# Optimization experiments

Measured on AMD Instinct MI355X. Metric: run time of the kernel, lower is better.

## Reference

```python
import jax, jax.numpy as jnp
import numpy as np

B, C, H, W = 4, 3, 96, 96
HW = H * W
IGNORE = 0          # HD_IGNORE_CLASS_INDEX
BIG = 1e9           # stand-in for +inf in masked min


def setup_inputs() -> dict:
    key = jax.random.key(0)
    k1, k2 = jax.random.split(key)
    predictions = jax.random.normal(k1, (B, C, H, W), dtype=jnp.float32)
    labels_int = jax.random.randint(k2, (B, H, W), 0, C, dtype=jnp.int32)
    return {"predictions": predictions, "labels_int": labels_int}


def get_boundary(img):
    # img: [B, C, H, W] binary mask. Faithful to the numpy version (square images):
    # new = img + 4-neighbor sums (zero outside), boundary = img * (5 - new).
    pad = lambda x, spec: jnp.pad(x, ((0, 0), (0, 0)) + spec)
    new = (img
           + pad(img[:, :, 1:, :], ((0, 1), (0, 0)))
           + pad(img[:, :, :-1, :], ((1, 0), (0, 0)))
           + pad(img[:, :, :, 1:], ((0, 0), (0, 1)))
           + pad(img[:, :, :, :-1], ((0, 0), (1, 0))))
    return img * (5.0 - new)


def _pixel_dist_matrix():
    yy, xx = jnp.meshgrid(jnp.arange(H), jnp.arange(W), indexing="ij")
    coords = jnp.stack([yy.ravel(), xx.ravel()], axis=-1).astype(jnp.float32)  # [HW,2] (row,col) like argwhere
    sq = jnp.sum(coords * coords, axis=-1)
    D2 = sq[:, None] + sq[None, :] - 2.0 * (coords @ coords.T)
    return jnp.sqrt(jnp.maximum(D2, 0.0))  # [HW, HW]


def reference(predictions, labels_int):
    labels = jax.nn.one_hot(labels_int, C, axis=1, dtype=jnp.float32)        # [B,C,H,W]
    preds = jax.nn.one_hot(jnp.argmax(predictions, axis=1), C, axis=1,
                           dtype=jnp.float32)                                # [B,C,H,W]

    bd_a = (get_boundary(preds) > 0).astype(jnp.float32)
    bd_b = (get_boundary(labels) > 0).astype(jnp.float32)

    a = preds.reshape(B * C, HW)
    b = labels.reshape(B * C, HW)
    ba = bd_a.reshape(B * C, HW)
    bb = bd_b.reshape(B * C, HW)

    D = _pixel_dist_matrix()  # [HW, HW], shared across all (batch, class) pairs

    def pair(args):
        a_, b_, ba_, bb_ = args
        n_a = a_.sum()
        n_b = b_.sum()
        a_fwd = a_ * (1.0 - b_)   # pred-only pixels (false positive region)
        b_bwd = b_ * (1.0 - a_)   # label-only pixels
        # min distance from every pixel to boundary set, via masked min (no argwhere)
        mins_f = jnp.min(jnp.where(bb_[None, :] > 0, D, BIG), axis=1)  # to boundary(b)
        mins_b = jnp.min(jnp.where(ba_[None, :] > 0, D, BIG), axis=1)  # to boundary(a)
        # mean(min) * |A_fwd| / |a| == sum(min over A_fwd) / |a|
        hd_f = jnp.where((a_fwd.sum() > 0) & (bb_.sum() > 0),
                         jnp.sum(a_fwd * mins_f) / jnp.maximum(n_a, 1.0), 0.0)
        hd_b = jnp.where((b_bwd.sum() > 0) & (ba_.sum() > 0),
                         jnp.sum(b_bwd * mins_b) / jnp.maximum(n_b, 1.0), 0.0)
        hd = jnp.maximum(hd_f, hd_b)
        # empty prediction mask -> failure case (ignore_failed_hd = False => (h+w)/4)
        hd = jnp.where(n_a > 0, hd, (H + W) / 4.0)
        return hd, (n_a == 0).astype(jnp.float32)

    hd_pairs, failed_pairs = jax.lax.map(pair, (a, b, ba, bb))

    hd = hd_pairs.reshape(B, C).at[:, IGNORE].set(0.0)
    failed = failed_pairs.reshape(B, C).sum(axis=0).at[IGNORE].set(0.0)

    HD = jnp.zeros((B, C + 2), dtype=jnp.float32)
    HD = HD.at[:, :C].set(hd)
    HD = HD.at[:, C].set(jnp.mean(hd, axis=1))            # HD[:, -2] = mean over all C classes
    HD = HD.at[:, C + 1].set(jnp.mean(hd[:, :C - 1], axis=1))  # HD[:, -1] = mean over first C-1 (faithful to [:-3])

    Fc = jnp.zeros((C + 2,), dtype=jnp.float32)
    Fc = Fc.at[:C].set(failed)
    Fc = Fc.at[C].set(jnp.mean(failed))
    Fc = Fc.at[C + 1].set(jnp.mean(failed[1:C]))
    return HD, Fc
```

## Files before the change

kernel.cpp:

```cpp
#include <hip/hip_runtime.h>
#include <math.h>

namespace {
constexpr int Bn = 4, Cn = 3, Hn = 96, Wn = 96;
constexpr int HWn = Hn * Wn;
constexpr int NP  = Bn * Cn;
constexpr int NBANDS = 3;
constexpr int NBLK1 = Bn * NBANDS;
constexpr int SENT = 62500;

constexpr int FLAG_WORDS = Bn * HWn / 4;
constexpr int CNT_OFF  = FLAG_WORDS;
constexpr int SUM_OFF  = ((CNT_OFF + NBLK1 * 8 + 15) / 16) * 16;
constexpr int SUM_WORDS = 2 * NP * 16;
constexpr int TICK_OFF = SUM_OFF + SUM_WORDS;
constexpr int ZERO_WORDS = SUM_WORDS + 16;
constexpr int MK_OFF   = TICK_OFF + 16;

__device__ __forceinline__ int SUMF_I(int pr) { return SUM_OFF + pr * 16; }
__device__ __forceinline__ int SUMB_I(int pr) { return SUM_OFF + (NP + pr) * 16; }
}

__global__ __launch_bounds__(384) void k_front(const float* __restrict__ preds,
                                               const int* __restrict__ labels,
                                               int* __restrict__ wi) {
    int blk = blockIdx.x, j = threadIdx.x;
    int b = blk / NBANDS, w = blk - b * NBANDS;
    int y0 = w * 32;
    const float* pb = preds + (size_t)b * Cn * HWn;
    const int*   lb = labels + b * HWn;

    __shared__ unsigned char apc[34 * 96];
    __shared__ unsigned char albl[34 * 96];
    __shared__ unsigned char aflg[32 * 96];
    __shared__ int scnt[6];

    if (j < 6) scnt[j] = 0;

    for (int t = j; t < 34 * 96; t += 384) {
        int r = t / 96, x = t - r * 96;
        int y = y0 - 1 + r;
        if ((unsigned)y < 96u) {
            int p = y * Wn + x;
            float v0 = pb[p], v1 = pb[HWn + p], v2 = pb[2 * HWn + p];
            int bi = 0; float bv = v0;
            if (v1 > bv) { bv = v1; bi = 1; }
            if (v2 > bv) { bv = v2; bi = 2; }
            apc[t]  = (unsigned char)bi;
            albl[t] = (unsigned char)lb[p];
        }
    }
    __syncthreads();

    int cA[3] = {0, 0, 0}, cB[3] = {0, 0, 0};
#pragma unroll
    for (int k = 0; k < 8; ++k) {
        int t = j + k * 384;
        int r = t / 96, x = t - r * 96;
        int y = y0 + r, ly = r + 1;
        int pc = apc[ly * 96 + x], l = albl[ly * 96 + x];
        int ca = 0, cb = 0;
        if (y > 0)  { ca += (apc[(ly - 1) * 96 + x] == pc); cb += (albl[(ly - 1) * 96 + x] == l); }
        if (y < 95) { ca += (apc[(ly + 1) * 96 + x] == pc); cb += (albl[(ly + 1) * 96 + x] == l); }
        if (x > 0)  { ca += (apc[ly * 96 + x - 1] == pc);   cb += (albl[ly * 96 + x - 1] == l); }
        if (x < 95) { ca += (apc[ly * 96 + x + 1] == pc);   cb += (albl[ly * 96 + x + 1] == l); }
        unsigned char f = (unsigned char)(pc | (l << 2) | ((ca < 4) << 4) | ((cb < 4) << 5));
        aflg[t] = f;
        ((unsigned char*)wi)[b * HWn + y * Wn + x] = f;
        cA[0] += (pc == 0); cA[1] += (pc == 1); cA[2] += (pc == 2);
        cB[0] += (l == 0);  cB[1] += (l == 1);  cB[2] += (l == 2);
    }
    int vals[6] = {cA[0], cA[1], cA[2], cB[0], cB[1], cB[2]};
#pragma unroll
    for (int q = 0; q < 6; ++q) {
        int v = vals[q];
#pragma unroll
        for (int off = 32; off >= 1; off >>= 1) v += __shfl_xor(v, off, 64);
        if ((j & 63) == 0) atomicAdd(&scnt[q], v);
    }
    __syncthreads();

    for (int k = j; k < 576; k += 384) {
        int c = k / 192, rem = k - c * 192;
        int which = rem / 96, x = rem - which * 96;
        unsigned m = 0;
#pragma unroll
        for (int r = 0; r < 32; ++r) {
            unsigned f = aflg[r * 96 + x];
            unsigned bit = (which == 0)
                ? (unsigned)(((f & 3) == (unsigned)c) & ((f >> 4) & 1))
                : (unsigned)((((f >> 2) & 3) == (unsigned)c) & ((f >> 5) & 1));
            m |= bit << r;
        }
        int pr = b * Cn + c;
        wi[MK_OFF + pr * 576 + (which ? (w + 3) : w) * 96 + x] = (int)m;
    }
    if (j < 6) wi[CNT_OFF + blk * 8 + j] = scnt[j];
    if (blk == 0) {
        if (j < ZERO_WORDS) wi[SUM_OFF + j] = 0;
        if (j + 384 < ZERO_WORDS) wi[SUM_OFF + j + 384] = 0;
    }
}

__global__ __launch_bounds__(384) void k_edt_sum(int* __restrict__ wi,
                                                 float* __restrict__ wf,
                                                 float* __restrict__ out) {
    int pr = blockIdx.y;
    int rb = blockIdx.x;
    int j  = threadIdx.x;
    int b = pr / Cn, c = pr - b * Cn;

    __shared__ unsigned int mlds[576];
    __shared__ unsigned int glds[384];
    __shared__ float sF6[6], sB6[6];
    __shared__ int lastflag;

    for (int k = j; k < 576; k += 384)
        mlds[k] = (unsigned int)wi[MK_OFF + pr * 576 + k];
    __syncthreads();

    int r = j / 96, xp = j - r * 96;
    int y = rb * 4 + r;

    unsigned long long alo = (unsigned long long)mlds[xp]
                           | ((unsigned long long)mlds[96 + xp] << 32);
    unsigned long long ahi = mlds[192 + xp];
    unsigned long long blo = (unsigned long long)mlds[288 + xp]
                           | ((unsigned long long)mlds[384 + xp] << 32);
    unsigned long long bhi = mlds[480 + xp];

    __uint128_t Ma = ((__uint128_t)ahi << 64) | alo;
    __uint128_t Mb = ((__uint128_t)bhi << 64) | blo;

    auto dist1d = [&](__uint128_t M) -> int {
        int du = 200, dd = 200;
        __uint128_t s = M >> y;
        if (s) {
            unsigned long long lo = (unsigned long long)s;
            du = lo ? __builtin_ctzll(lo) : 64 + __builtin_ctzll((unsigned long long)(s >> 64));
        }
        s = M << (127 - y);
        if (s) {
            unsigned long long h = (unsigned long long)(s >> 64);
            dd = h ? __builtin_clzll(h) : 64 + __builtin_clzll((unsigned long long)s);
        }
        int d = min(du, dd);
        return (d >= Hn) ? SENT : d * d;
    };
    glds[j] = (unsigned)dist1d(Mb) | ((unsigned)dist1d(Ma) << 16);
    __syncthreads();

    int p = y * Wn + xp;
    unsigned f = ((const unsigned char*)wi)[b * HWn + p];
    int a  = ((f & 3) == (unsigned)c);
    int bm = (((f >> 2) & 3) == (unsigned)c);
    int na = wi[CNT_OFF + (b * NBANDS + 0) * 8 + c]
           + wi[CNT_OFF + (b * NBANDS + 1) * 8 + c]
           + wi[CNT_OFF + (b * NBANDS + 2) * 8 + c];
    int nb = wi[CNT_OFF + (b * NBANDS + 0) * 8 + 3 + c]
           + wi[CNT_OFF + (b * NBANDS + 1) * 8 + 3 + c]
           + wi[CNT_OFF + (b * NBANDS + 2) * 8 + 3 + c];
    bool af = a && !bm && (nb > 0);
    bool bw = bm && !a && (na > 0);

    float s = 0.0f;
    if (af || bw) {
        int sh = af ? 0 : 16;
        int md2 = 0x7fffffff;
        const unsigned int* grow = &glds[r * 96];
#pragma unroll 8
        for (int q = 0; q < Wn; ++q) {
            int gs = (grow[q] >> sh) & 0xffff;
            int dx = xp - q;
            md2 = min(md2, gs + dx * dx);
        }
        s = sqrtf((float)md2);
    }
    float vF = af ? s : 0.0f;
    float vB = bw ? s : 0.0f;
#pragma unroll
    for (int off = 32; off >= 1; off >>= 1) {
        vF += __shfl_xor(vF, off, 64);
        vB += __shfl_xor(vB, off, 64);
    }
    int wv = j >> 6;
    if ((j & 63) == 0) { sF6[wv] = vF; sB6[wv] = vB; }
    __syncthreads();
    if (j == 0) {
        float t = sF6[0] + sF6[1] + sF6[2] + sF6[3] + sF6[4] + sF6[5];
        if (t != 0.0f) atomicAdd(&wf[SUMF_I(pr)], t);
    } else if (j == 64) {
        float t = sB6[0] + sB6[1] + sB6[2] + sB6[3] + sB6[4] + sB6[5];
        if (t != 0.0f) atomicAdd(&wf[SUMB_I(pr)], t);
    }

    __syncthreads();
    if (j == 0) {
        int old = atomicAdd(&wi[TICK_OFF], 1);
        lastflag = (old == NP * 24 - 1);
    }
    __syncthreads();
    if (!lastflag) return;

    __shared__ float hds[12];
    __shared__ float fld[12];
    if (j < 12) {
        int bb = j / Cn, cc = j - bb * Cn;
        int nA = wi[CNT_OFF + (bb * NBANDS + 0) * 8 + cc]
               + wi[CNT_OFF + (bb * NBANDS + 1) * 8 + cc]
               + wi[CNT_OFF + (bb * NBANDS + 2) * 8 + cc];
        int nB = wi[CNT_OFF + (bb * NBANDS + 0) * 8 + 3 + cc]
               + wi[CNT_OFF + (bb * NBANDS + 1) * 8 + 3 + cc]
               + wi[CNT_OFF + (bb * NBANDS + 2) * 8 + 3 + cc];
        float sFv = atomicAdd(&wf[SUMF_I(j)], 0.0f);
        float sBv = atomicAdd(&wf[SUMB_I(j)], 0.0f);
        float h, fl = 0.0f;
        if (nA == 0) { h = (Hn + Wn) / 4.0f; fl = 1.0f; }
        else {
            h = fmaxf(sFv / fmaxf((float)nA, 1.0f), sBv / fmaxf((float)nB, 1.0f));
        }
        if (cc == 0) { h = 0.0f; fl = 0.0f; }
        hds[j] = h; fld[j] = fl;
    }
    __syncthreads();
    if (j == 0) {
        float failed[3] = {0.f, 0.f, 0.f};
        for (int q = 0; q < 12; ++q) failed[q % 3] += fld[q];
        for (int bb = 0; bb < Bn; ++bb) {
            float* row = out + bb * (Cn + 2);
            float ssum = 0.f;
            for (int cc = 0; cc < Cn; ++cc) { row[cc] = hds[bb * 3 + cc]; ssum += row[cc]; }
            row[Cn]     = ssum / (float)Cn;
            row[Cn + 1] = (hds[bb * 3] + hds[bb * 3 + 1]) / (float)(Cn - 1);
        }
        float* Fc = out + Bn * (Cn + 2);
        float fs = 0.f;
        for (int cc = 0; cc < Cn; ++cc) { Fc[cc] = failed[cc]; fs += failed[cc]; }
        Fc[Cn]     = fs / (float)Cn;
        Fc[Cn + 1] = (failed[1] + failed[2]) / (float)(Cn - 1);
    }
}

extern "C" void kernel_launch(void* const* d_in, const int* in_sizes, int n_in,
                              void* d_out, int out_size, void* d_ws, size_t ws_size,
                              hipStream_t stream) {
    const float* preds  = (const float*)d_in[0];
    const int*   labels = (const int*)d_in[1];
    float* out = (float*)d_out;
    int*   wi = (int*)d_ws;
    float* wf = (float*)d_ws;

    k_front<<<NBLK1, 384, 0, stream>>>(preds, labels, wi);
    dim3 g2(Hn / 4, NP);
    k_edt_sum<<<g2, 384, 0, stream>>>(wi, wf, out);
}
```

Measured before the change: 74.80 us.

## Split front kernel into column chunks and share pixel counts via LDS

The front kernel now splits each 32-row band into four 24-column chunks, so it launches 48 blocks of 256 threads instead of 12 blocks of 384. Each block loads a 34x26 haloed tile, and fewer threads build the per-column boundary masks. The goal is more parallelism in a small, latency-bound first stage. In the second kernel, two threads sum the per-block counts into shared memory once, instead of every thread reading six global count words. The cost is more halo reloads across block edges, and the final reduction now reads 12 partial counts per (batch, class) pair.

```diff
diff --git a/kernel.cpp b/kernel.cpp
--- a/kernel.cpp
+++ b/kernel.cpp
@@ -6,7 +6,9 @@
 constexpr int HWn = Hn * Wn;
 constexpr int NP  = Bn * Cn;
 constexpr int NBANDS = 3;
-constexpr int NBLK1 = Bn * NBANDS;
+constexpr int NCHUNK = 4;
+constexpr int BPI   = NBANDS * NCHUNK;
+constexpr int NBLK1 = Bn * BPI;
 constexpr int SENT = 62500;
 
 constexpr int FLAG_WORDS = Bn * HWn / 4;
@@ -21,26 +23,27 @@
 __device__ __forceinline__ int SUMB_I(int pr) { return SUM_OFF + (NP + pr) * 16; }
 }
 
-__global__ __launch_bounds__(384) void k_front(const float* __restrict__ preds,
+__global__ __launch_bounds__(256) void k_front(const float* __restrict__ preds,
                                                const int* __restrict__ labels,
                                                int* __restrict__ wi) {
     int blk = blockIdx.x, j = threadIdx.x;
-    int b = blk / NBANDS, w = blk - b * NBANDS;
-    int y0 = w * 32;
+    int b = blk / BPI, rem = blk - b * BPI;
+    int w = rem / NCHUNK, q = rem - w * NCHUNK;
+    int y0 = w * 32, x0 = q * 24;
     const float* pb = preds + (size_t)b * Cn * HWn;
     const int*   lb = labels + b * HWn;
 
-    __shared__ unsigned char apc[34 * 96];
-    __shared__ unsigned char albl[34 * 96];
-    __shared__ unsigned char aflg[32 * 96];
+    __shared__ unsigned char apc[34 * 26];
+    __shared__ unsigned char albl[34 * 26];
+    __shared__ unsigned char aflg[32 * 24];
     __shared__ int scnt[6];
 
     if (j < 6) scnt[j] = 0;
 
-    for (int t = j; t < 34 * 96; t += 384) {
-        int r = t / 96, x = t - r * 96;
-        int y = y0 - 1 + r;
-        if ((unsigned)y < 96u) {
+    for (int t = j; t < 34 * 26; t += 256) {
+        int r = t / 26, xl = t - r * 26;
+        int y = y0 - 1 + r, x = x0 - 1 + xl;
+        if ((unsigned)y < 96u && (unsigned)x < 96u) {
             int p = y * Wn + x;
             float v0 = pb[p], v1 = pb[HWn + p], v2 = pb[2 * HWn + p];
             int bi = 0; float bv = v0;
@@ -54,16 +57,17 @@
 
     int cA[3] = {0, 0, 0}, cB[3] = {0, 0, 0};
 #pragma unroll
-    for (int k = 0; k < 8; ++k) {
-        int t = j + k * 384;
-        int r = t / 96, x = t - r * 96;
-        int y = y0 + r, ly = r + 1;
-        int pc = apc[ly * 96 + x], l = albl[ly * 96 + x];
+    for (int k = 0; k < 3; ++k) {
+        int t = j + k * 256;
+        int r = t / 24, xl = t - r * 24;
+        int y = y0 + r, x = x0 + xl;
+        int li = (r + 1) * 26 + (xl + 1);
+        int pc = apc[li], l = albl[li];
         int ca = 0, cb = 0;
-        if (y > 0)  { ca += (apc[(ly - 1) * 96 + x] == pc); cb += (albl[(ly - 1) * 96 + x] == l); }
-        if (y < 95) { ca += (apc[(ly + 1) * 96 + x] == pc); cb += (albl[(ly + 1) * 96 + x] == l); }
-        if (x > 0)  { ca += (apc[ly * 96 + x - 1] == pc);   cb += (albl[ly * 96 + x - 1] == l); }
-        if (x < 95) { ca += (apc[ly * 96 + x + 1] == pc);   cb += (albl[ly * 96 + x + 1] == l); }
+        if (y > 0)  { ca += (apc[li - 26] == pc); cb += (albl[li - 26] == l); }
+        if (y < 95) { ca += (apc[li + 26] == pc); cb += (albl[li + 26] == l); }
+        if (x > 0)  { ca += (apc[li - 1] == pc);  cb += (albl[li - 1] == l); }
+        if (x < 95) { ca += (apc[li + 1] == pc);  cb += (albl[li + 1] == l); }
         unsigned char f = (unsigned char)(pc | (l << 2) | ((ca < 4) << 4) | ((cb < 4) << 5));
         aflg[t] = f;
         ((unsigned char*)wi)[b * HWn + y * Wn + x] = f;
@@ -72,33 +76,33 @@
     }
     int vals[6] = {cA[0], cA[1], cA[2], cB[0], cB[1], cB[2]};
 #pragma unroll
-    for (int q = 0; q < 6; ++q) {
-        int v = vals[q];
+    for (int qq = 0; qq < 6; ++qq) {
+        int v = vals[qq];
 #pragma unroll
         for (int off = 32; off >= 1; off >>= 1) v += __shfl_xor(v, off, 64);
-        if ((j & 63) == 0) atomicAdd(&scnt[q], v);
-    }
-    __syncthreads();
-
-    for (int k = j; k < 576; k += 384) {
-        int c = k / 192, rem = k - c * 192;
-        int which = rem / 96, x = rem - which * 96;
+        if ((j & 63) == 0) atomicAdd(&scnt[qq], v);
+    }
+    __syncthreads();
+
+    if (j < 144) {
+        int c = j / 48, rem2 = j - c * 48;
+        int which = rem2 / 24, xl = rem2 - which * 24;
         unsigned m = 0;
 #pragma unroll
         for (int r = 0; r < 32; ++r) {
-            unsigned f = aflg[r * 96 + x];
+            unsigned f = aflg[r * 24 + xl];
             unsigned bit = (which == 0)
                 ? (unsigned)(((f & 3) == (unsigned)c) & ((f >> 4) & 1))
                 : (unsigned)((((f >> 2) & 3) == (unsigned)c) & ((f >> 5) & 1));
             m |= bit << r;
         }
         int pr = b * Cn + c;
-        wi[MK_OFF + pr * 576 + (which ? (w + 3) : w) * 96 + x] = (int)m;
+        wi[MK_OFF + pr * 576 + (which ? (w + 3) : w) * 96 + (x0 + xl)] = (int)m;
     }
     if (j < 6) wi[CNT_OFF + blk * 8 + j] = scnt[j];
     if (blk == 0) {
         if (j < ZERO_WORDS) wi[SUM_OFF + j] = 0;
-        if (j + 384 < ZERO_WORDS) wi[SUM_OFF + j + 384] = 0;
+        if (j + 256 < ZERO_WORDS) wi[SUM_OFF + j + 256] = 0;
     }
 }
 
@@ -113,10 +117,17 @@
     __shared__ unsigned int mlds[576];
     __shared__ unsigned int glds[384];
     __shared__ float sF6[6], sB6[6];
+    __shared__ int nab[2];
     __shared__ int lastflag;
 
     for (int k = j; k < 576; k += 384)
         mlds[k] = (unsigned int)wi[MK_OFF + pr * 576 + k];
+    if (j < 2) {
+        int s = 0;
+        for (int k = 0; k < BPI; ++k)
+            s += wi[CNT_OFF + (b * BPI + k) * 8 + j * 3 + c];
+        nab[j] = s;
+    }
     __syncthreads();
 
     int r = j / 96, xp = j - r * 96;
@@ -154,12 +165,7 @@
     unsigned f = ((const unsigned char*)wi)[b * HWn + p];
     int a  = ((f & 3) == (unsigned)c);
     int bm = (((f >> 2) & 3) == (unsigned)c);
-    int na = wi[CNT_OFF + (b * NBANDS + 0) * 8 + c]
-           + wi[CNT_OFF + (b * NBANDS + 1) * 8 + c]
-           + wi[CNT_OFF + (b * NBANDS + 2) * 8 + c];
-    int nb = wi[CNT_OFF + (b * NBANDS + 0) * 8 + 3 + c]
-           + wi[CNT_OFF + (b * NBANDS + 1) * 8 + 3 + c]
-           + wi[CNT_OFF + (b * NBANDS + 2) * 8 + 3 + c];
+    int na = nab[0], nb = nab[1];
     bool af = a && !bm && (nb > 0);
     bool bw = bm && !a && (na > 0);
 
@@ -206,12 +212,11 @@
     __shared__ float fld[12];
     if (j < 12) {
         int bb = j / Cn, cc = j - bb * Cn;
-        int nA = wi[CNT_OFF + (bb * NBANDS + 0) * 8 + cc]
-               + wi[CNT_OFF + (bb * NBANDS + 1) * 8 + cc]
-               + wi[CNT_OFF + (bb * NBANDS + 2) * 8 + cc];
-        int nB = wi[CNT_OFF + (bb * NBANDS + 0) * 8 + 3 + cc]
-               + wi[CNT_OFF + (bb * NBANDS + 1) * 8 + 3 + cc]
-               + wi[CNT_OFF + (bb * NBANDS + 2) * 8 + 3 + cc];
+        int nA = 0, nB = 0;
+        for (int k = 0; k < BPI; ++k) {
+            nA += wi[CNT_OFF + (bb * BPI + k) * 8 + cc];
+            nB += wi[CNT_OFF + (bb * BPI + k) * 8 + 3 + cc];
+        }
         float sFv = atomicAdd(&wf[SUMF_I(j)], 0.0f);
         float sBv = atomicAdd(&wf[SUMB_I(j)], 0.0f);
         float h, fl = 0.0f;
@@ -250,7 +255,7 @@
     int*   wi = (int*)d_ws;
     float* wf = (float*)d_ws;
 
-    k_front<<<NBLK1, 384, 0, stream>>>(preds, labels, wi);
+    k_front<<<NBLK1, 256, 0, stream>>>(preds, labels, wi);
     dim3 g2(Hn / 4, NP);
     k_edt_sum<<<g2, 384, 0, stream>>>(wi, wf, out);
 }
```

Result: faster. 71.54 us (-4.4%).
